# Kernel optimization log

Hardware: AMD Instinct MI355X
Metric: run time of the kernel (lower is better)

## Reference

```python
import jax, jax.numpy as jnp
import numpy as np

N = 4096

def _backsub(rel_bounds):
    # rel_bounds: list; first entry is ((n,1),(n,1)) input bounds, rest are
    # (out, in+1) relative-bound matrices. Returns exact abs bounds (n,1).
    cur_lb, cur_ub = rel_bounds[-1]
    for prev_lb, prev_ub in reversed(rel_bounds[:-1]):
        bias_row = jnp.zeros((1, prev_lb.shape[-1]), prev_lb.dtype).at[0, -1].set(1.0)
        plb = jnp.concatenate([prev_lb, bias_row], axis=0)
        pub = jnp.concatenate([prev_ub, bias_row], axis=0)
        wp, wn = jax.nn.relu(cur_lb), jax.nn.relu(-cur_lb)
        new_lb = wp @ plb - wn @ pub
        wp, wn = jax.nn.relu(cur_ub), jax.nn.relu(-cur_ub)
        new_ub = wp @ pub - wn @ plb
        cur_lb, cur_ub = new_lb, new_ub
    return cur_lb, cur_ub


def setup_inputs() -> dict:
    key = jax.random.key(0)
    k = jax.random.split(key, 7)
    base = jax.random.normal(k[0], (N, 1), jnp.float32)
    eps = 0.1
    lb0 = base - eps
    ub0 = base + eps
    scale = 0.02  # keep bound magnitudes realistic through the matmul chain
    W1_lb = jax.random.normal(k[1], (N, N + 1), jnp.float32) * scale
    W1_ub = W1_lb + jnp.abs(jax.random.normal(k[2], (N, N + 1), jnp.float32)) * 0.001
    W2_lb = jax.random.normal(k[3], (N, N + 1), jnp.float32) * scale
    W2_ub = W2_lb + jnp.abs(jax.random.normal(k[4], (N, N + 1), jnp.float32)) * 0.001
    alphas = jax.random.uniform(k[5], (N,), jnp.float32)
    return {"lb0": lb0, "ub0": ub0, "W1_lb": W1_lb, "W1_ub": W1_ub,
            "W2_lb": W2_lb, "W2_ub": W2_ub, "alphas": alphas}


def reference(lb0, ub0, W1_lb, W1_ub, W2_lb, W2_ub, alphas):
    prev_lb, prev_ub = _backsub([(lb0, ub0), (W1_lb, W1_ub), (W2_lb, W2_ub)])  # (N,1)
    lb_s = prev_lb[:, 0]
    ub_s = prev_ub[:, 0]
    n = lb_s.shape[0]
    dt = prev_lb.dtype

    alpha = jnp.clip(alphas, 0.0, 1.0)
    alpha = jnp.where(lb_s > 0.0, jnp.ones((), dt), alpha)
    alpha = jnp.where(ub_s <= 0.0, jnp.zeros((), dt), alpha)
    current_lb = jnp.concatenate([jnp.diag(alpha), jnp.zeros((n, 1), dt)], axis=1)

    feps = jnp.finfo(dt).eps
    slope_ub = prev_ub / (prev_ub - prev_lb + feps)          # (N,1)
    slope_ub = jnp.where(prev_lb > 0.0, jnp.ones((), dt), slope_ub)
    slope_ub = jnp.where(prev_ub < 0.0, jnp.zeros((), dt), slope_ub)
    bias_ub = -prev_lb * slope_ub
    bias_ub = jnp.where((prev_lb > 0.0) | (prev_ub < 0.0), jnp.zeros((), dt), bias_ub)
    current_ub = jnp.concatenate([jnp.diag(slope_ub[:, 0]), bias_ub], axis=1)

    # stacked rel_bound appended by the layer: [0]=lower, [1]=upper, each (N, N+1)
    return jnp.stack([current_lb, current_ub])
```

## Files before the change

### kernel.cpp

```cpp
#include <hip/hip_runtime.h>
#include <float.h>

#define N4K 4096
#define NP1 4097

typedef __attribute__((ext_vector_type(4))) float f32x4;
typedef __attribute__((ext_vector_type(8))) short bf16x8;

__device__ __forceinline__ unsigned short f2bf(float x) {
    union { float f; unsigned int u; } v; v.f = x;
    unsigned int r = v.u + 0x7FFFu + ((v.u >> 16) & 1u);
    return (unsigned short)(r >> 16);
}

__device__ __forceinline__ void gload_lds16(const void* g, void* l) {
    __builtin_amdgcn_global_load_lds(
        (const __attribute__((address_space(1))) unsigned int*)g,
        (__attribute__((address_space(3))) unsigned int*)l,
        16, 0, 0);
}

__device__ __forceinline__ void bar() {
    asm volatile("" ::: "memory");
    __builtin_amdgcn_s_barrier();
    asm volatile("" ::: "memory");
}

__global__ __launch_bounds__(256) void prep_A2(const float* __restrict__ W2lb,
                                               const float* __restrict__ W2ub,
                                               const float* __restrict__ mb,
                                               const float* __restrict__ db,
                                               unsigned short* __restrict__ Abf,
                                               float* __restrict__ prev) {
    int b = blockIdx.x;
    int chain = b >> 12, i = b & 4095;
    const float* row = (chain ? W2ub : W2lb) + (long long)i * NP1;
    unsigned short* abf_row = Abf + ((long long)chain << 24) + (long long)i * N4K;
    float s = chain ? 1.f : -1.f;
    float part = 0.f;
#pragma unroll 4
    for (int p = 0; p < 16; ++p) {
        int k = threadIdx.x + p * 256;
        float wv = row[k];
        abf_row[k] = f2bf(wv);
        part += wv * mb[k] + s * db[k] * fabsf(wv);
    }
    __shared__ float red[4];
#pragma unroll
    for (int off = 32; off; off >>= 1) part += __shfl_down(part, off);
    if ((threadIdx.x & 63) == 0) red[threadIdx.x >> 6] = part;
    __syncthreads();
    if (threadIdx.x == 0)
        prev[b] = red[0] + red[1] + red[2] + red[3] + row[4096];
}

__global__ __launch_bounds__(256) void prep_B(const float* __restrict__ W1lb,
                                              const float* __restrict__ W1ub,
                                              unsigned short* __restrict__ Bmt,
                                              unsigned short* __restrict__ Bdt) {
    __shared__ unsigned short Lm[64 * 65];
    __shared__ unsigned short Ld[64 * 65];
    int j0 = blockIdx.x * 64, k0 = blockIdx.y * 64;
    int t = threadIdx.x;
    int jj = t & 63, kkb = t >> 6;
#pragma unroll 4
    for (int p = 0; p < 16; ++p) {
        int kk = kkb + p * 4;
        long long off = (long long)(k0 + kk) * NP1 + j0 + jj;
        float l = W1lb[off], u = W1ub[off];
        Lm[kk * 65 + jj] = f2bf(0.5f * (l + u));
        Ld[kk * 65 + jj] = f2bf(0.5f * (u - l));
    }
    __syncthreads();
#pragma unroll
    for (int p = 0; p < 2; ++p) {
        int jl = p * 32 + (t >> 3);
        int kl = (t & 7) * 8;
        bf16x8 vm, vd;
#pragma unroll
        for (int i = 0; i < 8; ++i) {
            vm[i] = (short)Lm[(kl + i) * 65 + jl];
            vd[i] = (short)Ld[(kl + i) * 65 + jl];
        }
        *(bf16x8*)&Bmt[(long long)(j0 + jl) * N4K + k0 + kl] = vm;
        *(bf16x8*)&Bdt[(long long)(j0 + jl) * N4K + k0 + kl] = vd;
    }
}

__global__ __launch_bounds__(256) void prep_mbdb(const float* __restrict__ W1lb,
                                                 const float* __restrict__ W1ub,
                                                 float* __restrict__ mb,
                                                 float* __restrict__ db) {
    int k = blockIdx.x * 256 + threadIdx.x;
    if (k < N4K) {
        float l = W1lb[(long long)k * NP1 + 4096];
        float u = W1ub[(long long)k * NP1 + 4096];
        mb[k] = 0.5f * (l + u);
        db[k] = 0.5f * (u - l);
    }
}

__global__ __launch_bounds__(512, 2) void gemm_fused(const unsigned short* __restrict__ Abf,
                                                     const unsigned short* __restrict__ Bmt,
                                                     const unsigned short* __restrict__ Bdt,
                                                     const float* __restrict__ lb0,
                                                     const float* __restrict__ ub0,
                                                     float* __restrict__ prev) {
    __shared__ unsigned short As[2][16384];
    __shared__ unsigned short Bms[2][8192];
    __shared__ unsigned short Bds[2][8192];

    int wg = blockIdx.x;
    int swz = (wg & 7) * 128 + (wg >> 3);
    int rt = swz & 31;
    int ct = swz >> 5;

    int chain = rt >> 4;
    const unsigned short* Aptr = Abf + ((long long)chain << 24) + (long long)(rt & 15) * 256 * N4K;
    const unsigned short* Bmp = Bmt + (long long)ct * 128 * N4K;
    const unsigned short* Bdp = Bdt + (long long)ct * 128 * N4K;

    int tid = threadIdx.x;
    int lane = tid & 63, w = tid >> 6;
    int wr = w >> 1, wc = w & 1;
    int la = lane & 15, kq = lane >> 4;
    int x7 = la & 7;

    int srow = tid >> 3;
    int sce = ((tid & 7) ^ (srow & 7)) << 3;
    const unsigned short* aS = Aptr + (long long)srow * N4K + sce;
    const unsigned short* mS = Bmp + (long long)srow * N4K + sce;
    const unsigned short* dS = Bdp + (long long)srow * N4K + sce;
    const long long R64 = 64LL * N4K;
    unsigned ldst = w * 512;

    int arow = wr * 64 + la;
    int brow = wc * 64 + la;

    f32x4 acc[4][4];
#pragma unroll
    for (int m = 0; m < 4; ++m)
#pragma unroll
        for (int n = 0; n < 4; ++n) acc[m][n] = (f32x4){0.f, 0.f, 0.f, 0.f};

#pragma unroll
    for (int q = 0; q < 4; ++q) gload_lds16(aS + q * R64, &As[0][q * 4096 + ldst]);
#pragma unroll
    for (int q = 0; q < 2; ++q) gload_lds16(mS + q * R64, &Bms[0][q * 4096 + ldst]);
#pragma unroll
    for (int q = 0; q < 2; ++q) gload_lds16(dS + q * R64, &Bds[0][q * 4096 + ldst]);
    asm volatile("s_waitcnt vmcnt(0)" ::: "memory");
    bar();

#define FRAG(arr, cur, rb, f, k) \
    (*(const bf16x8*)&arr[cur][((rb) + (f) * 16) * 64 + ((((k) * 4 + kq) ^ x7) * 8)])

#pragma unroll 1
    for (int t = 0; t < 64; ++t) {
        const int cur = t & 1, nxt = cur ^ 1;
        const int k0n = (t + 1) * 64;
        const bool pf = (t < 63);

        bf16x8 af[4][2], ax[4][2], bd0[2][2], bd1[2][2], bm0[2][2], bm1[2][2];

#pragma unroll
        for (int m = 0; m < 4; ++m)
#pragma unroll
            for (int k = 0; k < 2; ++k) af[m][k] = FRAG(As, cur, arow, m, k);
#pragma unroll
        for (int n = 0; n < 2; ++n)
#pragma unroll
            for (int k = 0; k < 2; ++k) bd0[n][k] = FRAG(Bds, cur, brow, n, k);
#pragma unroll
        for (int m = 0; m < 4; ++m)
#pragma unroll
            for (int k = 0; k < 2; ++k)
                ax[m][k] = chain ? (af[m][k] & (short)0x7FFF) : (af[m][k] | (short)0x8000);
        if (pf) {
            gload_lds16(dS + k0n, &Bds[nxt][ldst]);
            gload_lds16(dS + R64 + k0n, &Bds[nxt][4096 + ldst]);
        }
        bar();
        __builtin_amdgcn_s_setprio(1);
#pragma unroll
        for (int m = 0; m < 4; ++m)
#pragma unroll
            for (int n = 0; n < 2; ++n)
#pragma unroll
                for (int k = 0; k < 2; ++k)
                    acc[m][n] = __builtin_amdgcn_mfma_f32_16x16x32_bf16(ax[m][k], bd0[n][k], acc[m][n], 0, 0, 0);
        __builtin_amdgcn_s_setprio(0);
        bar();

#pragma unroll
        for (int n = 0; n < 2; ++n)
#pragma unroll
            for (int k = 0; k < 2; ++k) bd1[n][k] = FRAG(Bds, cur, brow, n + 2, k);
        if (pf) {
            gload_lds16(aS + k0n, &As[nxt][ldst]);
            gload_lds16(aS + R64 + k0n, &As[nxt][4096 + ldst]);
        }
        bar();
        __builtin_amdgcn_s_setprio(1);
#pragma unroll
        for (int m = 0; m < 4; ++m)
#pragma unroll
            for (int n = 0; n < 2; ++n)
#pragma unroll
                for (int k = 0; k < 2; ++k)
                    acc[m][n + 2] = __builtin_amdgcn_mfma_f32_16x16x32_bf16(ax[m][k], bd1[n][k], acc[m][n + 2], 0, 0, 0);
        __builtin_amdgcn_s_setprio(0);
        if (pf) asm volatile("s_waitcnt vmcnt(4)" ::: "memory");
        else    asm volatile("s_waitcnt vmcnt(0)" ::: "memory");
        bar();

#pragma unroll
        for (int n = 0; n < 2; ++n)
#pragma unroll
            for (int k = 0; k < 2; ++k) bm0[n][k] = FRAG(Bms, cur, brow, n, k);
        if (pf) {
            gload_lds16(aS + 2 * R64 + k0n, &As[nxt][8192 + ldst]);
            gload_lds16(aS + 3 * R64 + k0n, &As[nxt][12288 + ldst]);
        }
        bar();
        __builtin_amdgcn_s_setprio(1);
#pragma unroll
        for (int m = 0; m < 4; ++m)
#pragma unroll
            for (int n = 0; n < 2; ++n)
#pragma unroll
                for (int k = 0; k < 2; ++k)
                    acc[m][n] = __builtin_amdgcn_mfma_f32_16x16x32_bf16(af[m][k], bm0[n][k], acc[m][n], 0, 0, 0);
        __builtin_amdgcn_s_setprio(0);
        bar();

#pragma unroll
        for (int n = 0; n < 2; ++n)
#pragma unroll
            for (int k = 0; k < 2; ++k) bm1[n][k] = FRAG(Bms, cur, brow, n + 2, k);
        if (pf) {
            gload_lds16(mS + k0n, &Bms[nxt][ldst]);
            gload_lds16(mS + R64 + k0n, &Bms[nxt][4096 + ldst]);
        }
        bar();
        __builtin_amdgcn_s_setprio(1);
#pragma unroll
        for (int m = 0; m < 4; ++m)
#pragma unroll
            for (int n = 0; n < 2; ++n)
#pragma unroll
                for (int k = 0; k < 2; ++k)
                    acc[m][n + 2] = __builtin_amdgcn_mfma_f32_16x16x32_bf16(af[m][k], bm1[n][k], acc[m][n + 2], 0, 0, 0);
        __builtin_amdgcn_s_setprio(0);
        if (pf) asm volatile("s_waitcnt vmcnt(2)" ::: "memory");
        bar();
    }
#undef FRAG

    float s = chain ? 1.f : -1.f;
    float rowpart[4][4];
#pragma unroll
    for (int m = 0; m < 4; ++m)
#pragma unroll
        for (int r = 0; r < 4; ++r) rowpart[m][r] = 0.f;

    int jbase = ct * 128 + wc * 64;
#pragma unroll
    for (int n = 0; n < 4; ++n) {
        int j = jbase + n * 16 + la;
        float l0 = lb0[j], u0 = ub0[j];
        float mj = 0.5f * (l0 + u0);
        float sdj = s * 0.5f * (u0 - l0);
#pragma unroll
        for (int m = 0; m < 4; ++m)
#pragma unroll
            for (int r = 0; r < 4; ++r) {
                float v = acc[m][n][r];
                rowpart[m][r] += v * mj + sdj * fabsf(v);
            }
    }
    long long rowg = (long long)chain * N4K + (rt & 15) * 256 + wr * 64 + kq * 4;
#pragma unroll
    for (int m = 0; m < 4; ++m)
#pragma unroll
        for (int r = 0; r < 4; ++r) {
            float v = rowpart[m][r];
            v += __shfl_xor(v, 1);
            v += __shfl_xor(v, 2);
            v += __shfl_xor(v, 4);
            v += __shfl_xor(v, 8);
            if (la == 0) atomicAdd(&prev[rowg + m * 16 + r], v);
        }
}

__global__ __launch_bounds__(256) void epilogue(const float* __restrict__ prev,
                                                const float* __restrict__ alphas,
                                                float* __restrict__ out) {
    int i = blockIdx.x * 256 + threadIdx.x;
    if (i >= N4K) return;
    float lb = prev[i], ub = prev[N4K + i];
    float a = fminf(fmaxf(alphas[i], 0.f), 1.f);
    if (lb > 0.f) a = 1.f;
    if (ub <= 0.f) a = 0.f;
    float slope = ub / (ub - lb + FLT_EPSILON);
    if (lb > 0.f) slope = 1.f;
    if (ub < 0.f) slope = 0.f;
    float bias = -lb * slope;
    if (lb > 0.f || ub < 0.f) bias = 0.f;
    long long P = NP1, half = (long long)N4K * NP1;
    out[(long long)i * P + i] = a;
    out[half + (long long)i * P + i] = slope;
    out[half + (long long)i * P + 4096] = bias;
}

extern "C" void kernel_launch(void* const* d_in, const int* in_sizes, int n_in,
                              void* d_out, int out_size, void* d_ws, size_t ws_size,
                              hipStream_t stream) {
    const float* lb0    = (const float*)d_in[0];
    const float* ub0    = (const float*)d_in[1];
    const float* W1lb   = (const float*)d_in[2];
    const float* W1ub   = (const float*)d_in[3];
    const float* W2lb   = (const float*)d_in[4];
    const float* W2ub   = (const float*)d_in[5];
    const float* alphas = (const float*)d_in[6];

    char* ws = (char*)d_ws;
    float* prev = (float*)ws;
    float* mb   = (float*)(ws + 32768);
    float* db   = (float*)(ws + 49152);
    unsigned short* Abf = (unsigned short*)(ws + 65536);
    unsigned short* Bmt = (unsigned short*)(ws + 65536 + 67108864);
    unsigned short* Bdt = (unsigned short*)(ws + 65536 + 100663296);
    size_t need = 65536ULL + 67108864ULL + 2ULL * 33554432ULL;
    if (ws_size < need) return;

    (void)hipMemsetAsync(d_out, 0, (size_t)out_size * 4, stream);

    prep_mbdb<<<16, 256, 0, stream>>>(W1lb, W1ub, mb, db);
    prep_A2<<<8192, 256, 0, stream>>>(W2lb, W2ub, mb, db, Abf, prev);
    prep_B<<<dim3(64, 64), 256, 0, stream>>>(W1lb, W1ub, Bmt, Bdt);
    gemm_fused<<<1024, 512, 0, stream>>>(Abf, Bmt, Bdt, lb0, ub0, prev);
    epilogue<<<16, 256, 0, stream>>>(prev, alphas, (float*)d_out);
}
```

Baseline: 716.5 us.

## Reorder GEMM main loop by k-half and replace atomics with partial-sum reduction

The inner loop of the fused GEMM is regrouped so that each phase handles one k-half across all four n-fragments, rather than two n-fragments across both k-halves. This lets the loop drop the extra barrier in each of the four phases, leaving one barrier per phase instead of two. The final per-row atomicAdds are replaced by plain stores of per-column-slice partials into a scratch area of the output buffer. A new small reduce kernel sums those partials plus the bias term, and a second memset then re-zeroes the borrowed output region. This removes atomic contention and barrier stalls, but adds a kernel launch and a 2 MB memset, and relies on the fewer barriers still being enough to avoid LDS races.

```diff
diff --git a/kernel.cpp b/kernel.cpp
--- a/kernel.cpp
+++ b/kernel.cpp
@@ -31,7 +31,7 @@
                                                const float* __restrict__ mb,
                                                const float* __restrict__ db,
                                                unsigned short* __restrict__ Abf,
-                                               float* __restrict__ prev) {
+                                               float* __restrict__ bias_part) {
     int b = blockIdx.x;
     int chain = b >> 12, i = b & 4095;
     const float* row = (chain ? W2ub : W2lb) + (long long)i * NP1;
@@ -51,7 +51,7 @@
     if ((threadIdx.x & 63) == 0) red[threadIdx.x >> 6] = part;
     __syncthreads();
     if (threadIdx.x == 0)
-        prev[b] = red[0] + red[1] + red[2] + red[3] + row[4096];
+        bias_part[b] = red[0] + red[1] + red[2] + red[3] + row[4096];
 }
 
 __global__ __launch_bounds__(256) void prep_B(const float* __restrict__ W1lb,
@@ -105,7 +105,7 @@
                                                      const unsigned short* __restrict__ Bdt,
                                                      const float* __restrict__ lb0,
                                                      const float* __restrict__ ub0,
-                                                     float* __restrict__ prev) {
+                                                     float* __restrict__ pp) {
     __shared__ unsigned short As[2][16384];
     __shared__ unsigned short Bms[2][8192];
     __shared__ unsigned short Bds[2][8192];
@@ -161,96 +161,77 @@
         const int k0n = (t + 1) * 64;
         const bool pf = (t < 63);
 
-        bf16x8 af[4][2], ax[4][2], bd0[2][2], bd1[2][2], bm0[2][2], bm1[2][2];
-
-#pragma unroll
-        for (int m = 0; m < 4; ++m)
-#pragma unroll
-            for (int k = 0; k < 2; ++k) af[m][k] = FRAG(As, cur, arow, m, k);
-#pragma unroll
-        for (int n = 0; n < 2; ++n)
-#pragma unroll
-            for (int k = 0; k < 2; ++k) bd0[n][k] = FRAG(Bds, cur, brow, n, k);
-#pragma unroll
-        for (int m = 0; m < 4; ++m)
-#pragma unroll
-            for (int k = 0; k < 2; ++k)
-                ax[m][k] = chain ? (af[m][k] & (short)0x7FFF) : (af[m][k] | (short)0x8000);
+        bf16x8 a0[4], a1[4], ax0[4], ax1[4], bd0[4], bd1[4], bm0[4], bm1[4];
+
+#pragma unroll
+        for (int m = 0; m < 4; ++m) a0[m] = FRAG(As, cur, arow, m, 0);
+#pragma unroll
+        for (int n = 0; n < 4; ++n) bd0[n] = FRAG(Bds, cur, brow, n, 0);
         if (pf) {
             gload_lds16(dS + k0n, &Bds[nxt][ldst]);
             gload_lds16(dS + R64 + k0n, &Bds[nxt][4096 + ldst]);
         }
-        bar();
+#pragma unroll
+        for (int m = 0; m < 4; ++m)
+            ax0[m] = chain ? (a0[m] & (short)0x7FFF) : (a0[m] | (short)0x8000);
         __builtin_amdgcn_s_setprio(1);
 #pragma unroll
         for (int m = 0; m < 4; ++m)
 #pragma unroll
-            for (int n = 0; n < 2; ++n)
-#pragma unroll
-                for (int k = 0; k < 2; ++k)
-                    acc[m][n] = __builtin_amdgcn_mfma_f32_16x16x32_bf16(ax[m][k], bd0[n][k], acc[m][n], 0, 0, 0);
+            for (int n = 0; n < 4; ++n)
+                acc[m][n] = __builtin_amdgcn_mfma_f32_16x16x32_bf16(ax0[m], bd0[n], acc[m][n], 0, 0, 0);
         __builtin_amdgcn_s_setprio(0);
         bar();
 
 #pragma unroll
-        for (int n = 0; n < 2; ++n)
-#pragma unroll
-            for (int k = 0; k < 2; ++k) bd1[n][k] = FRAG(Bds, cur, brow, n + 2, k);
+        for (int m = 0; m < 4; ++m) a1[m] = FRAG(As, cur, arow, m, 1);
+#pragma unroll
+        for (int n = 0; n < 4; ++n) bd1[n] = FRAG(Bds, cur, brow, n, 1);
         if (pf) {
             gload_lds16(aS + k0n, &As[nxt][ldst]);
             gload_lds16(aS + R64 + k0n, &As[nxt][4096 + ldst]);
         }
-        bar();
+#pragma unroll
+        for (int m = 0; m < 4; ++m)
+            ax1[m] = chain ? (a1[m] & (short)0x7FFF) : (a1[m] | (short)0x8000);
         __builtin_amdgcn_s_setprio(1);
 #pragma unroll
         for (int m = 0; m < 4; ++m)
 #pragma unroll
-            for (int n = 0; n < 2; ++n)
-#pragma unroll
-                for (int k = 0; k < 2; ++k)
-                    acc[m][n + 2] = __builtin_amdgcn_mfma_f32_16x16x32_bf16(ax[m][k], bd1[n][k], acc[m][n + 2], 0, 0, 0);
+            for (int n = 0; n < 4; ++n)
+                acc[m][n] = __builtin_amdgcn_mfma_f32_16x16x32_bf16(ax1[m], bd1[n], acc[m][n], 0, 0, 0);
         __builtin_amdgcn_s_setprio(0);
         if (pf) asm volatile("s_waitcnt vmcnt(4)" ::: "memory");
         else    asm volatile("s_waitcnt vmcnt(0)" ::: "memory");
         bar();
 
 #pragma unroll
-        for (int n = 0; n < 2; ++n)
-#pragma unroll
-            for (int k = 0; k < 2; ++k) bm0[n][k] = FRAG(Bms, cur, brow, n, k);
+        for (int n = 0; n < 4; ++n) bm0[n] = FRAG(Bms, cur, brow, n, 0);
         if (pf) {
             gload_lds16(aS + 2 * R64 + k0n, &As[nxt][8192 + ldst]);
             gload_lds16(aS + 3 * R64 + k0n, &As[nxt][12288 + ldst]);
         }
-        bar();
         __builtin_amdgcn_s_setprio(1);
 #pragma unroll
         for (int m = 0; m < 4; ++m)
 #pragma unroll
-            for (int n = 0; n < 2; ++n)
-#pragma unroll
-                for (int k = 0; k < 2; ++k)
-                    acc[m][n] = __builtin_amdgcn_mfma_f32_16x16x32_bf16(af[m][k], bm0[n][k], acc[m][n], 0, 0, 0);
+            for (int n = 0; n < 4; ++n)
+                acc[m][n] = __builtin_amdgcn_mfma_f32_16x16x32_bf16(a0[m], bm0[n], acc[m][n], 0, 0, 0);
         __builtin_amdgcn_s_setprio(0);
         bar();
 
 #pragma unroll
-        for (int n = 0; n < 2; ++n)
-#pragma unroll
-            for (int k = 0; k < 2; ++k) bm1[n][k] = FRAG(Bms, cur, brow, n + 2, k);
+        for (int n = 0; n < 4; ++n) bm1[n] = FRAG(Bms, cur, brow, n, 1);
         if (pf) {
             gload_lds16(mS + k0n, &Bms[nxt][ldst]);
             gload_lds16(mS + R64 + k0n, &Bms[nxt][4096 + ldst]);
         }
-        bar();
         __builtin_amdgcn_s_setprio(1);
 #pragma unroll
         for (int m = 0; m < 4; ++m)
 #pragma unroll
-            for (int n = 0; n < 2; ++n)
-#pragma unroll
-                for (int k = 0; k < 2; ++k)
-                    acc[m][n + 2] = __builtin_amdgcn_mfma_f32_16x16x32_bf16(af[m][k], bm1[n][k], acc[m][n + 2], 0, 0, 0);
+            for (int n = 0; n < 4; ++n)
+                acc[m][n] = __builtin_amdgcn_mfma_f32_16x16x32_bf16(a1[m], bm1[n], acc[m][n], 0, 0, 0);
         __builtin_amdgcn_s_setprio(0);
         if (pf) asm volatile("s_waitcnt vmcnt(2)" ::: "memory");
         bar();
@@ -280,6 +261,7 @@
             }
     }
     long long rowg = (long long)chain * N4K + (rt & 15) * 256 + wr * 64 + kq * 4;
+    long long slice = (long long)(ct * 2 + wc) * 8192;
 #pragma unroll
     for (int m = 0; m < 4; ++m)
 #pragma unroll
@@ -289,8 +271,18 @@
             v += __shfl_xor(v, 2);
             v += __shfl_xor(v, 4);
             v += __shfl_xor(v, 8);
-            if (la == 0) atomicAdd(&prev[rowg + m * 16 + r], v);
-        }
+            if (la == 0) pp[slice + rowg + m * 16 + r] = v;
+        }
+}
+
+__global__ __launch_bounds__(256) void reduce_pp(const float* __restrict__ pp,
+                                                 const float* __restrict__ bias_part,
+                                                 float* __restrict__ prev) {
+    int j = blockIdx.x * 256 + threadIdx.x;
+    float s = bias_part[j];
+#pragma unroll 8
+    for (int c = 0; c < 64; ++c) s += pp[(long long)c * 8192 + j];
+    prev[j] = s;
 }
 
 __global__ __launch_bounds__(256) void epilogue(const float* __restrict__ prev,
@@ -325,20 +317,25 @@
     const float* alphas = (const float*)d_in[6];
 
     char* ws = (char*)d_ws;
-    float* prev = (float*)ws;
+    float* bias_part = (float*)ws;
     float* mb   = (float*)(ws + 32768);
     float* db   = (float*)(ws + 49152);
+    float* prev = (float*)(ws + 32768);
     unsigned short* Abf = (unsigned short*)(ws + 65536);
     unsigned short* Bmt = (unsigned short*)(ws + 65536 + 67108864);
     unsigned short* Bdt = (unsigned short*)(ws + 65536 + 100663296);
     size_t need = 65536ULL + 67108864ULL + 2ULL * 33554432ULL;
     if (ws_size < need) return;
 
+    float* pp = (float*)d_out;
+
     (void)hipMemsetAsync(d_out, 0, (size_t)out_size * 4, stream);
 
     prep_mbdb<<<16, 256, 0, stream>>>(W1lb, W1ub, mb, db);
-    prep_A2<<<8192, 256, 0, stream>>>(W2lb, W2ub, mb, db, Abf, prev);
+    prep_A2<<<8192, 256, 0, stream>>>(W2lb, W2ub, mb, db, Abf, bias_part);
     prep_B<<<dim3(64, 64), 256, 0, stream>>>(W1lb, W1ub, Bmt, Bdt);
-    gemm_fused<<<1024, 512, 0, stream>>>(Abf, Bmt, Bdt, lb0, ub0, prev);
+    gemm_fused<<<1024, 512, 0, stream>>>(Abf, Bmt, Bdt, lb0, ub0, pp);
+    reduce_pp<<<32, 256, 0, stream>>>(pp, bias_part, prev);
+    (void)hipMemsetAsync(d_out, 0, 64 * 8192 * 4, stream);
     epilogue<<<16, 256, 0, stream>>>(prev, alphas, (float*)d_out);
 }
```

Result: faster. 668.8 us (-6.7%).
